# Kernel tuning notes

Measured on AMD Instinct MI355X. Metric: run time of the kernel, lower is better.

Reference implementation:

```python
import jax, jax.numpy as jnp
import numpy as np

B, S, D, H = 8, 1024, 256, 8


def setup_inputs() -> dict:
    key = jax.random.key(0)
    ks = jax.random.split(key, 8)
    scale = 0.02
    return {
        "x": jax.random.normal(ks[0], (B, S, D), dtype=jnp.float32),
        "Wq": jax.random.normal(ks[1], (H, D, D), dtype=jnp.float32) * scale,
        "Wk": jax.random.normal(ks[2], (H, D, D), dtype=jnp.float32) * scale,
        "Wv": jax.random.normal(ks[3], (H, D, D), dtype=jnp.float32) * scale,
        "bq": jax.random.normal(ks[4], (H, D), dtype=jnp.float32) * scale,
        "bk": jax.random.normal(ks[5], (H, D), dtype=jnp.float32) * scale,
        "bv": jax.random.normal(ks[6], (H, D), dtype=jnp.float32) * scale,
        "Wp": jax.random.normal(ks[7], (D, H * D), dtype=jnp.float32) * scale,
    }


def reference(x, Wq, Wk, Wv, bq, bk, bv, Wp):
    # Per-head Linear layers, vectorized over the head axis.
    # torch Linear: y = x @ W.T + b, W shape [out, in] -> einsum 'bsd,hed->bhse'
    q = jnp.einsum('bsd,hed->bhse', x, Wq) + bq[:, None, :]   # [B,H,S,D]
    k = jnp.einsum('bsd,hed->bhse', x, Wk) + bk[:, None, :]
    v = jnp.einsum('bsd,hed->bhse', x, Wv) + bv[:, None, :]
    d = x.shape[-1]
    scores = jnp.einsum('bhse,bhte->bhst', q, k) / jnp.sqrt(jnp.float32(d))
    attn = jax.nn.softmax(scores, axis=-1)                    # softmax over keys (dim=2 per head)
    o = jnp.einsum('bhst,bhte->bhse', attn, v)                # [B,H,S,D]
    # concat heads along feature dim (head order preserved)
    o = o.transpose(0, 2, 1, 3).reshape(x.shape[0], x.shape[1], -1)  # [B,S,H*D]
    return o @ Wp.T                                           # bias-free projection [B,S,D]
```

## Files before the change

kernel.cpp:

```cpp
#include <hip/hip_runtime.h>

typedef unsigned short u16;
typedef __attribute__((ext_vector_type(4)))  float f32x4;
typedef __attribute__((ext_vector_type(16))) float f32x16;
typedef __attribute__((ext_vector_type(8)))  short s16x8;
typedef __attribute__((ext_vector_type(4)))  unsigned short u16x4;
typedef __attribute__((ext_vector_type(8)))  unsigned short u16x8;

typedef const __attribute__((address_space(1))) void* gp1;
typedef __attribute__((address_space(3))) void* lp3;
#define GLOAD16(g, l) __builtin_amdgcn_global_load_lds((gp1)(g), (lp3)(l), 16, 0, 0)

__device__ __forceinline__ u16 f2bf(float f) {
    union { float f; unsigned u; } c; c.f = f;
    unsigned r = c.u + 0x7fffu + ((c.u >> 16) & 1u);
    return (u16)(r >> 16);
}

__global__ void castall(const float* __restrict__ x,  const float* __restrict__ wq,
                        const float* __restrict__ wk, const float* __restrict__ wv,
                        const float* __restrict__ wp,
                        u16* __restrict__ xb,  u16* __restrict__ wqb, u16* __restrict__ wkb,
                        u16* __restrict__ wvb, u16* __restrict__ wpb) {
    int blk = blockIdx.x;
    const float* src; u16* dst; long off;
    if (blk < 2048) { src = x; dst = xb; off = (long)blk * 1024; }
    else {
        int w = (blk - 2048) >> 9, bb = (blk - 2048) & 511;
        src = (w == 0 ? wq : w == 1 ? wk : w == 2 ? wv : wp);
        dst = (w == 0 ? wqb : w == 1 ? wkb : w == 2 ? wvb : wpb);
        off = (long)bb * 1024;
    }
    long i = off + threadIdx.x * 4;
    f32x4 v = *(const f32x4*)(src + i);
    u16x4 o;
    o[0] = f2bf(v[0]); o[1] = f2bf(v[1]); o[2] = f2bf(v[2]); o[3] = f2bf(v[3]);
    *(u16x4*)(dst + i) = o;
}

__global__ __launch_bounds__(256) void qkv_gemm(
    const u16* __restrict__ xb,
    const u16* __restrict__ Wqb, const u16* __restrict__ Wkb, const u16* __restrict__ Wvb,
    const float* __restrict__ bq, const float* __restrict__ bk, const float* __restrict__ bv,
    u16* __restrict__ Qb, u16* __restrict__ Kimg, u16* __restrict__ Vimg)
{
    __shared__ u16 smem[32768];
    u16* As = smem;
    u16* Bs = smem + 16384;
    const int tid  = threadIdx.x;
    const int lane = tid & 63;
    const int li   = lane & 15, lg = lane >> 4;
    const int wave = tid >> 6;
    const int wr   = wave >> 1, wc = wave & 1;
    const int m0   = blockIdx.x * 128;
    const int n0g  = blockIdx.y * 128;
    const int w    = n0g >> 11;
    const int h    = (n0g >> 8) & 7;
    const int e0   = n0g & 255;
    const u16* Wsel = (w == 0 ? Wqb : (w == 1 ? Wkb : Wvb)) + h * 65536;

    f32x4 acc[4][4] = {};

    for (int k0 = 0; k0 < 256; k0 += 128) {
        __syncthreads();
        #pragma unroll
        for (int p = 0; p < 8; ++p) {
            const int g = p * 256 + tid, row = g >> 4, cl = g & 15;
            const size_t soff = ((size_t)row) * 256 + k0 + ((cl ^ (row & 7)) * 8);
            GLOAD16(&xb[(size_t)m0 * 256 + soff],   &As[g * 8]);
            GLOAD16(&Wsel[(size_t)e0 * 256 + soff], &Bs[g * 8]);
        }
        __syncthreads();

        #pragma unroll
        for (int kk = 0; kk < 4; ++kk) {
            s16x8 af[4], bf[4];
            #pragma unroll
            for (int mi = 0; mi < 4; ++mi) {
                const int arow = wr * 64 + mi * 16 + li;
                af[mi] = *(const s16x8*)&As[arow * 128 + (((kk * 4 + lg) ^ (arow & 7)) * 8)];
            }
            #pragma unroll
            for (int ni = 0; ni < 4; ++ni) {
                const int brow = wc * 64 + ni * 16 + li;
                bf[ni] = *(const s16x8*)&Bs[brow * 128 + (((kk * 4 + lg) ^ (brow & 7)) * 8)];
            }
            #pragma unroll
            for (int mi = 0; mi < 4; ++mi)
                #pragma unroll
                for (int ni = 0; ni < 4; ++ni)
                    acc[mi][ni] = __builtin_amdgcn_mfma_f32_16x16x32_bf16(af[mi], bf[ni], acc[mi][ni], 0, 0, 0);
        }
    }

    const int b  = m0 >> 10;
    const int s0 = m0 & 1023;
    if (w == 0) {
        const float* bp = bq + 256 * h;
        #pragma unroll
        for (int ni = 0; ni < 4; ++ni) {
            const int e = e0 + wc * 64 + ni * 16 + li;
            const float bias = bp[e];
            u16* obase = Qb + ((size_t)(b * 8 + h)) * 1024 * 256 + e;
            #pragma unroll
            for (int mi = 0; mi < 4; ++mi)
                #pragma unroll
                for (int r = 0; r < 4; ++r) {
                    int s = s0 + wr * 64 + mi * 16 + lg * 4 + r;
                    obase[(size_t)s * 256] = f2bf(acc[mi][ni][r] + bias);
                }
        }
    } else if (w == 1) {
        const float* bp = bk + 256 * h;
        u16* kb = Kimg + ((size_t)(b * 8 + h)) * 262144;
        #pragma unroll
        for (int ni = 0; ni < 4; ++ni) {
            const int e = e0 + wc * 64 + ni * 16 + li;
            const float bias = bp[e];
            #pragma unroll
            for (int mi = 0; mi < 4; ++mi)
                #pragma unroll
                for (int r = 0; r < 4; ++r) {
                    int s = s0 + wr * 64 + mi * 16 + lg * 4 + r;
                    int t = s >> 5, rr = s & 31;
                    size_t idx = (size_t)t * 8192 + rr * 256
                               + (((e & ~7) ^ ((rr & 7) << 3)) | (e & 7));
                    kb[idx] = f2bf(acc[mi][ni][r] + bias);
                }
        }
    } else {
        const float* bp = bv + 256 * h;
        u16* vb = Vimg + ((size_t)(b * 8 + h)) * 327680;
        const int t0 = s0 >> 5;
        u16* Vt = smem;
        __syncthreads();
        #pragma unroll
        for (int ni = 0; ni < 4; ++ni) {
            const int eloc = wc * 64 + ni * 16 + li;
            const float bias = bp[e0 + eloc];
            #pragma unroll
            for (int mi = 0; mi < 4; ++mi) {
                const int sloc = wr * 64 + mi * 16 + lg * 4;
                u16x4 pk;
                #pragma unroll
                for (int r = 0; r < 4; ++r) pk[r] = f2bf(acc[mi][ni][r] + bias);
                *(u16x4*)&Vt[eloc * 132 + sloc] = pk;
            }
        }
        __syncthreads();
        #pragma unroll
        for (int p = 0; p < 8; ++p) {
            const int g    = p * 256 + tid;
            const int eloc = g >> 4;
            const int tt   = (g >> 2) & 3;
            const int ch   = g & 3;
            const int sloc = tt * 32 + ch * 8;
            u16x8 v = *(const u16x8*)&Vt[eloc * 132 + sloc];
            *(u16x8*)&vb[(size_t)(t0 + tt) * 10240 + (size_t)(e0 + eloc) * 40 + ch * 8] = v;
        }
    }
}

__device__ __forceinline__ void softmax_pack(
    f32x16& sacc, float& m_run, float& l_run, f32x16* oacc,
    int hi, s16x8& paA, s16x8& paB)
{
    const float C = 0.09016844f;
    const float THR = 16.0f;
    float pm = -1e30f;
    #pragma unroll
    for (int r = 0; r < 16; ++r) pm = fmaxf(pm, sacc[r]);
    pm = fmaxf(pm, __shfl_xor(pm, 32));
    if (!__all(pm - m_run <= THR)) {
        const float mnew = fmaxf(m_run, pm);
        const float corr = __builtin_amdgcn_exp2f((m_run - mnew) * C);
        l_run *= corr;
        #pragma unroll
        for (int r = 0; r < 16; ++r) {
            float rc = __shfl(corr, (r & 3) + 8 * (r >> 2) + 4 * hi);
            #pragma unroll
            for (int et = 0; et < 8; ++et) oacc[et][r] *= rc;
        }
        m_run = mnew;
    }
    float psum = 0.f;
    #pragma unroll
    for (int r = 0; r < 16; ++r) {
        float p = __builtin_amdgcn_exp2f((sacc[r] - m_run) * C);
        psum += p;
        sacc[r] = p;
    }
    psum += __shfl_xor(psum, 32);
    l_run += psum;
    unsigned dwA[4], dwB[4];
    #pragma unroll
    for (int c = 0; c < 4; ++c) {
        asm("v_cvt_pk_bf16_f32 %0, %1, %2" : "=v"(dwA[c]) : "v"(sacc[4*c]),   "v"(sacc[4*c+1]));
        asm("v_cvt_pk_bf16_f32 %0, %1, %2" : "=v"(dwB[c]) : "v"(sacc[4*c+2]), "v"(sacc[4*c+3]));
    }
    {
        unsigned a0 = dwA[0], a1 = dwA[1], b0 = dwB[0], b1 = dwB[1];
        asm("v_permlane32_swap_b32 %0, %1" : "+v"(a0), "+v"(a1));
        asm("v_permlane32_swap_b32 %0, %1" : "+v"(b0), "+v"(b1));
        union { unsigned u[4]; s16x8 v; } pk;
        pk.u[0] = a0; pk.u[1] = b0; pk.u[2] = a1; pk.u[3] = b1;
        paA = pk.v;
    }
    {
        unsigned a0 = dwA[2], a1 = dwA[3], b0 = dwB[2], b1 = dwB[3];
        asm("v_permlane32_swap_b32 %0, %1" : "+v"(a0), "+v"(a1));
        asm("v_permlane32_swap_b32 %0, %1" : "+v"(b0), "+v"(b1));
        union { unsigned u[4]; s16x8 v; } pk;
        pk.u[0] = a0; pk.u[1] = b0; pk.u[2] = a1; pk.u[3] = b1;
        paB = pk.v;
    }
}

__global__ __launch_bounds__(512, 2) void attn(
    const u16* __restrict__ Qb, const u16* __restrict__ Kimg,
    const u16* __restrict__ Vimg, u16* __restrict__ Ob)
{
    __shared__ u16 kbuf[3][8192];
    __shared__ u16 vbuf[3][10240];
    const int tid  = threadIdx.x;
    const int lane = tid & 63;
    const int wave = tid >> 6;
    const int col  = lane & 31;
    const int hi   = lane >> 5;
    const int hi8  = hi * 8;
    const int ksw  = (lane & 7) << 3;
    const int bid  = ((blockIdx.x & 7) << 5) | (blockIdx.x >> 3);
    const int bh   = bid >> 2;
    const int qblk = bid & 3;
    const int q0   = qblk * 256 + wave * 32;

    const u16* qp = Qb + ((size_t)bh * 1024 + q0) * 256;
    const u16* kg = Kimg + (size_t)bh * 262144;
    const u16* vg = Vimg + (size_t)bh * 327680;

    #define STAGE(sl, t)                                                          \
        {                                                                         \
            const int sl_ = (sl);                                                 \
            const int t_  = (t);                                                  \
            if (tid < 256) {                                                      \
                const size_t kb_ = (size_t)t_ * 8192 + tid * 8;                   \
                _Pragma("unroll")                                                 \
                for (int c_ = 0; c_ < 4; ++c_)                                    \
                    GLOAD16(&kg[kb_ + c_ * 2048], &kbuf[sl_][c_ * 2048 + tid * 8]); \
            } else {                                                              \
                const int    vt_ = tid - 256;                                     \
                const size_t vb_ = (size_t)t_ * 10240 + vt_ * 8;                  \
                _Pragma("unroll")                                                 \
                for (int c_ = 0; c_ < 5; ++c_)                                    \
                    GLOAD16(&vg[vb_ + c_ * 2048], &vbuf[sl_][c_ * 2048 + vt_ * 8]); \
            }                                                                     \
        }

    s16x8 qf[16];
    #pragma unroll
    for (int dk = 0; dk < 16; ++dk)
        qf[dk] = *(const s16x8*)&qp[(size_t)col * 256 + dk * 16 + hi8];

    STAGE(0, 0);
    STAGE(1, 1);
    STAGE(2, 2);

    f32x16 oacc[8] = {};
    float m_run = -1e30f, l_run = 0.f;
    f32x16 sacc;
    s16x8 paA, paB;

    for (int i = 0; i < 32; ++i) {
        if (tid < 256) { asm volatile("s_waitcnt vmcnt(8)"  ::: "memory"); }
        else           { asm volatile("s_waitcnt vmcnt(10)" ::: "memory"); }
        __builtin_amdgcn_s_barrier();
        asm volatile("" ::: "memory");
        const int slot = i % 3;
        const u16* kt = kbuf[slot];
        const u16* vt = vbuf[slot];

        __builtin_amdgcn_s_setprio(1);
        {
            sacc = (f32x16){};
            const int rb_ = col * 256;
            #pragma unroll
            for (int dk_ = 0; dk_ < 16; ++dk_) {
                s16x8 kf = *(const s16x8*)&kt[rb_ + ((dk_ * 16 + hi8) ^ ksw)];
                sacc = __builtin_amdgcn_mfma_f32_32x32x16_bf16(kf, qf[dk_], sacc, 0, 0, 0);
            }
        }
        __builtin_amdgcn_s_setprio(0);

        softmax_pack(sacc, m_run, l_run, oacc, hi, paA, paB);

        __builtin_amdgcn_s_setprio(1);
        {
            #pragma unroll
            for (int et_ = 0; et_ < 8; ++et_) {
                s16x8 vf = *(const s16x8*)&vt[(et_ * 32 + col) * 40 + hi8];
                oacc[et_] = __builtin_amdgcn_mfma_f32_32x32x16_bf16(paA, vf, oacc[et_], 0, 0, 0);
            }
            #pragma unroll
            for (int et_ = 0; et_ < 8; ++et_) {
                s16x8 vf = *(const s16x8*)&vt[(et_ * 32 + col) * 40 + 16 + hi8];
                oacc[et_] = __builtin_amdgcn_mfma_f32_32x32x16_bf16(paB, vf, oacc[et_], 0, 0, 0);
            }
        }
        __builtin_amdgcn_s_setprio(0);

        asm volatile("" ::: "memory");
        __builtin_amdgcn_s_barrier();
        asm volatile("" ::: "memory");
        const int nt = (i + 3 < 32) ? (i + 3) : 31;
        STAGE(slot, nt);
    }
    #undef STAGE

    const float linv = 1.0f / l_run;
    const int b = bh >> 3, h = bh & 7;
    u16* op = Ob + ((size_t)b * 1024) * 2048 + h * 256;
    #pragma unroll
    for (int r = 0; r < 16; ++r) {
        const int crow = (r & 3) + 8 * (r >> 2) + 4 * hi;
        float lr = __shfl(linv, crow);
        const size_t row = q0 + crow;
        #pragma unroll
        for (int et = 0; et < 8; ++et)
            op[row * 2048 + et * 32 + col] = f2bf(oacc[et][r] * lr);
    }
}

__global__ __launch_bounds__(256) void out_gemm(
    const u16* __restrict__ Ob, const u16* __restrict__ Wpb, float* __restrict__ out)
{
    __shared__ u16 As[32 * 128];
    __shared__ u16 Bs[128 * 128];
    const int tid  = threadIdx.x;
    const int lane = tid & 63;
    const int li   = lane & 15, lg = lane >> 4;
    const int wave = tid >> 6;
    const int wr   = wave >> 1, wc = wave & 1;
    const int m0   = blockIdx.x * 32;
    const int n0   = blockIdx.y * 128;

    f32x4 acc[4] = {};

    for (int k0 = 0; k0 < 2048; k0 += 128) {
        __syncthreads();
        #pragma unroll
        for (int p = 0; p < 2; ++p) {
            const int g = p * 256 + tid, row = g >> 4, cl = g & 15;
            GLOAD16(&Ob[(size_t)(m0 + row) * 2048 + k0 + ((cl ^ (row & 7)) * 8)],
                    &As[g * 8]);
        }
        #pragma unroll
        for (int p = 0; p < 8; ++p) {
            const int g = p * 256 + tid, row = g >> 4, cl = g & 15;
            GLOAD16(&Wpb[(size_t)(n0 + row) * 2048 + k0 + ((cl ^ (row & 7)) * 8)],
                    &Bs[g * 8]);
        }
        __syncthreads();

        const int arow = wr * 16 + li;
        s16x8 af[4];
        #pragma unroll
        for (int kk = 0; kk < 4; ++kk)
            af[kk] = *(const s16x8*)&As[arow * 128 + (((kk * 4 + lg) ^ (arow & 7)) * 8)];
        #pragma unroll
        for (int ni = 0; ni < 4; ++ni) {
            const int brow = wc * 64 + ni * 16 + li;
            #pragma unroll
            for (int kk = 0; kk < 4; ++kk) {
                s16x8 bf = *(const s16x8*)&Bs[brow * 128 + (((kk * 4 + lg) ^ (brow & 7)) * 8)];
                acc[ni] = __builtin_amdgcn_mfma_f32_16x16x32_bf16(af[kk], bf, acc[ni], 0, 0, 0);
            }
        }
    }

    #pragma unroll
    for (int ni = 0; ni < 4; ++ni) {
        int n = n0 + wc * 64 + ni * 16 + li;
        #pragma unroll
        for (int r = 0; r < 4; ++r) {
            int m = m0 + wr * 16 + lg * 4 + r;
            out[(size_t)m * 256 + n] = acc[ni][r];
        }
    }
}

extern "C" void kernel_launch(void* const* d_in, const int* in_sizes, int n_in,
                              void* d_out, int out_size, void* d_ws, size_t ws_size,
                              hipStream_t stream) {
    const float* x  = (const float*)d_in[0];
    const float* Wq = (const float*)d_in[1];
    const float* Wk = (const float*)d_in[2];
    const float* Wv = (const float*)d_in[3];
    const float* bq = (const float*)d_in[4];
    const float* bk = (const float*)d_in[5];
    const float* bv = (const float*)d_in[6];
    const float* Wp = (const float*)d_in[7];
    float* out = (float*)d_out;

    u16* xb   = (u16*)d_ws;
    u16* Wqb  = xb   + (1u << 21);
    u16* Wkb  = Wqb  + (1u << 19);
    u16* Wvb  = Wkb  + (1u << 19);
    u16* Wpb  = Wvb  + (1u << 19);
    u16* Qb   = Wpb  + (1u << 19);
    u16* Kimg = Qb   + (1u << 24);
    u16* Vimg = Kimg + (1u << 24);
    u16* Ob   = Vimg + 20971520u;

    castall<<<4096, 256, 0, stream>>>(x, Wq, Wk, Wv, Wp, xb, Wqb, Wkb, Wvb, Wpb);
    qkv_gemm<<<dim3(64, 48), 256, 0, stream>>>(xb, Wqb, Wkb, Wvb, bq, bk, bv, Qb, Kimg, Vimg);
    attn<<<256, 512, 0, stream>>>(Qb, Kimg, Vimg, Ob);
    out_gemm<<<dim3(256, 2), 256, 0, stream>>>(Ob, Wpb, out);
}
```

Before: 151.7 us.

## Skew half the waves by one tile so QK overlaps softmax/PV

Waves 4-7 now compute QK for tile i while running softmax and PV for tile i-1. Waves 0-3 keep the original in-order schedule, so MFMA-heavy and VALU-heavy phases of the two halves interleave on the CU. The V buffer grows from three to four slots so the lagging waves can still read V of the previous tile while the next tile is prefetched. An epilogue drains the last tile for the skewed waves. The cost is more LDS (about 128KB), some extra code and registers to carry the pending scores.

```diff
diff --git a/kernel.cpp b/kernel.cpp
--- a/kernel.cpp
+++ b/kernel.cpp
@@ -216,12 +216,45 @@
     }
 }
 
+__device__ __forceinline__ void qk_compute(
+    const u16* __restrict__ kt, const s16x8 (&qf)[16],
+    int col, int hi8, int ksw, f32x16& sacc)
+{
+    sacc = (f32x16){};
+    const int rb_ = col * 256;
+    __builtin_amdgcn_s_setprio(1);
+    #pragma unroll
+    for (int dk = 0; dk < 16; ++dk) {
+        s16x8 kf = *(const s16x8*)&kt[rb_ + ((dk * 16 + hi8) ^ ksw)];
+        sacc = __builtin_amdgcn_mfma_f32_32x32x16_bf16(kf, qf[dk], sacc, 0, 0, 0);
+    }
+    __builtin_amdgcn_s_setprio(0);
+}
+
+__device__ __forceinline__ void pv_compute(
+    const u16* __restrict__ vt, int col, int hi8,
+    const s16x8& paA, const s16x8& paB, f32x16* oacc)
+{
+    __builtin_amdgcn_s_setprio(1);
+    #pragma unroll
+    for (int et = 0; et < 8; ++et) {
+        s16x8 vf = *(const s16x8*)&vt[(et * 32 + col) * 40 + hi8];
+        oacc[et] = __builtin_amdgcn_mfma_f32_32x32x16_bf16(paA, vf, oacc[et], 0, 0, 0);
+    }
+    #pragma unroll
+    for (int et = 0; et < 8; ++et) {
+        s16x8 vf = *(const s16x8*)&vt[(et * 32 + col) * 40 + 16 + hi8];
+        oacc[et] = __builtin_amdgcn_mfma_f32_32x32x16_bf16(paB, vf, oacc[et], 0, 0, 0);
+    }
+    __builtin_amdgcn_s_setprio(0);
+}
+
 __global__ __launch_bounds__(512, 2) void attn(
     const u16* __restrict__ Qb, const u16* __restrict__ Kimg,
     const u16* __restrict__ Vimg, u16* __restrict__ Ob)
 {
     __shared__ u16 kbuf[3][8192];
-    __shared__ u16 vbuf[3][10240];
+    __shared__ u16 vbuf[4][10240];
     const int tid  = threadIdx.x;
     const int lane = tid & 63;
     const int wave = tid >> 6;
@@ -238,21 +271,22 @@
     const u16* kg = Kimg + (size_t)bh * 262144;
     const u16* vg = Vimg + (size_t)bh * 327680;
 
-    #define STAGE(sl, t)                                                          \
+    #define STAGE(ksl, vsl, t)                                                    \
         {                                                                         \
-            const int sl_ = (sl);                                                 \
             const int t_  = (t);                                                  \
             if (tid < 256) {                                                      \
+                const int ks_ = (ksl);                                            \
                 const size_t kb_ = (size_t)t_ * 8192 + tid * 8;                   \
                 _Pragma("unroll")                                                 \
                 for (int c_ = 0; c_ < 4; ++c_)                                    \
-                    GLOAD16(&kg[kb_ + c_ * 2048], &kbuf[sl_][c_ * 2048 + tid * 8]); \
+                    GLOAD16(&kg[kb_ + c_ * 2048], &kbuf[ks_][c_ * 2048 + tid * 8]); \
             } else {                                                              \
+                const int vs_ = (vsl);                                            \
                 const int    vt_ = tid - 256;                                     \
                 const size_t vb_ = (size_t)t_ * 10240 + vt_ * 8;                  \
                 _Pragma("unroll")                                                 \
                 for (int c_ = 0; c_ < 5; ++c_)                                    \
-                    GLOAD16(&vg[vb_ + c_ * 2048], &vbuf[sl_][c_ * 2048 + vt_ * 8]); \
+                    GLOAD16(&vg[vb_ + c_ * 2048], &vbuf[vs_][c_ * 2048 + vt_ * 8]); \
             }                                                                     \
         }
 
@@ -261,13 +295,13 @@
     for (int dk = 0; dk < 16; ++dk)
         qf[dk] = *(const s16x8*)&qp[(size_t)col * 256 + dk * 16 + hi8];
 
-    STAGE(0, 0);
-    STAGE(1, 1);
-    STAGE(2, 2);
+    STAGE(0, 0, 0);
+    STAGE(1, 1, 1);
+    STAGE(2, 2, 2);
 
     f32x16 oacc[8] = {};
     float m_run = -1e30f, l_run = 0.f;
-    f32x16 sacc;
+    f32x16 sprev;
     s16x8 paA, paB;
 
     for (int i = 0; i < 32; ++i) {
@@ -275,46 +309,35 @@
         else           { asm volatile("s_waitcnt vmcnt(10)" ::: "memory"); }
         __builtin_amdgcn_s_barrier();
         asm volatile("" ::: "memory");
-        const int slot = i % 3;
-        const u16* kt = kbuf[slot];
-        const u16* vt = vbuf[slot];
-
-        __builtin_amdgcn_s_setprio(1);
-        {
-            sacc = (f32x16){};
-            const int rb_ = col * 256;
-            #pragma unroll
-            for (int dk_ = 0; dk_ < 16; ++dk_) {
-                s16x8 kf = *(const s16x8*)&kt[rb_ + ((dk_ * 16 + hi8) ^ ksw)];
-                sacc = __builtin_amdgcn_mfma_f32_32x32x16_bf16(kf, qf[dk_], sacc, 0, 0, 0);
+        const u16* kt = kbuf[i % 3];
+
+        if (wave < 4) {
+            const u16* vt = vbuf[i & 3];
+            f32x16 sacc;
+            qk_compute(kt, qf, col, hi8, ksw, sacc);
+            softmax_pack(sacc, m_run, l_run, oacc, hi, paA, paB);
+            pv_compute(vt, col, hi8, paA, paB, oacc);
+        } else {
+            if (i > 0) {
+                softmax_pack(sprev, m_run, l_run, oacc, hi, paA, paB);
+                const u16* vt = vbuf[(i + 3) & 3];
+                pv_compute(vt, col, hi8, paA, paB, oacc);
             }
-        }
-        __builtin_amdgcn_s_setprio(0);
-
-        softmax_pack(sacc, m_run, l_run, oacc, hi, paA, paB);
-
-        __builtin_amdgcn_s_setprio(1);
-        {
-            #pragma unroll
-            for (int et_ = 0; et_ < 8; ++et_) {
-                s16x8 vf = *(const s16x8*)&vt[(et_ * 32 + col) * 40 + hi8];
-                oacc[et_] = __builtin_amdgcn_mfma_f32_32x32x16_bf16(paA, vf, oacc[et_], 0, 0, 0);
-            }
-            #pragma unroll
-            for (int et_ = 0; et_ < 8; ++et_) {
-                s16x8 vf = *(const s16x8*)&vt[(et_ * 32 + col) * 40 + 16 + hi8];
-                oacc[et_] = __builtin_amdgcn_mfma_f32_32x32x16_bf16(paB, vf, oacc[et_], 0, 0, 0);
-            }
-        }
-        __builtin_amdgcn_s_setprio(0);
+            qk_compute(kt, qf, col, hi8, ksw, sprev);
+        }
 
         asm volatile("" ::: "memory");
         __builtin_amdgcn_s_barrier();
         asm volatile("" ::: "memory");
         const int nt = (i + 3 < 32) ? (i + 3) : 31;
-        STAGE(slot, nt);
+        STAGE(i % 3, (i + 3) & 3, nt);
     }
     #undef STAGE
+
+    if (wave >= 4) {
+        softmax_pack(sprev, m_run, l_run, oacc, hi, paA, paB);
+        pv_compute(vbuf[3], col, hi8, paA, paB, oacc);
+    }
 
     const float linv = 1.0f / l_run;
     const int b = bh >> 3, h = bh & 7;
```

New measurement: 166.3 us. 1.1x slower.
